# Performance work log

Measured on AMD Instinct MI355X. Metric: run time of the kernel, lower is better.

The kernel has to match this reference:

```python
import jax, jax.numpy as jnp
from jax import lax
import numpy as np

# Surrogate spike: heaviside forward, fast-sigmoid surrogate gradient (standard SNN choice).
_SURROGATE_ALPHA = 10.0

@jax.custom_vjp
def surrogate_spike(x):
    return (x > 0).astype(x.dtype)

def _ss_fwd(x):
    return (x > 0).astype(x.dtype), x

def _ss_bwd(x, g):
    return (g / (1.0 + _SURROGATE_ALPHA * jnp.abs(x)) ** 2,)

surrogate_spike.defvjp(_ss_fwd, _ss_bwd)

B, C, T, R, TIME_BINS = 256, 64, 2048, 16, 128


def setup_inputs() -> dict:
    key = jax.random.key(0)
    ks = jax.random.split(key, 8)
    return {
        "transmit_spikes": jax.random.uniform(ks[0], (B, C, T), dtype=jnp.float32),
        "receive_spikes": jax.random.uniform(ks[1], (B, 2, C, T), dtype=jnp.float32),
        "conv_w": jax.random.normal(ks[2], (R, 3), dtype=jnp.float32) * 0.5,
        "conv_b": jax.random.normal(ks[3], (R,), dtype=jnp.float32) * 0.1,
        "frequency": jnp.linspace(-1.5, 1.5, R, dtype=jnp.float32),
        "decay": jax.random.normal(ks[4], (R,), dtype=jnp.float32) * 0.5,
        "threshold": jax.random.normal(ks[5], (R,), dtype=jnp.float32) * 0.5,
        "transmit_weight": jax.random.normal(ks[6], (), dtype=jnp.float32) * 0.1,
        "receive_weight": jax.random.normal(ks[7], (), dtype=jnp.float32) * 0.1,
    }


def reference(transmit_spikes, receive_spikes, conv_w, conv_b,
              frequency, decay, threshold, transmit_weight, receive_weight):
    # ---- _build_traces ----
    transmit = transmit_spikes.sum(axis=1)                        # (B, T)
    left = receive_spikes[:, 0].sum(axis=1)                       # (B, T)
    right = receive_spikes[:, 1].sum(axis=1)                      # (B, T)
    receive = 0.5 * (left + right)
    azimuth = left - right
    channel_axis = jnp.linspace(-1.0, 1.0, C).reshape(1, 1, C, 1)
    elevation = (receive_spikes * channel_axis).sum(axis=(1, 2))  # (B, T)
    signed_distance = (jax.nn.softplus(receive_weight) * receive
                       - jax.nn.softplus(transmit_weight) * transmit)
    traces = jnp.stack([signed_distance, azimuth, elevation], axis=1)  # (B, 3, T)
    # adaptive_avg_pool1d(T -> TIME_BINS); T divisible by TIME_BINS -> windowed mean
    traces = traces.reshape(B, 3, TIME_BINS, T // TIME_BINS).mean(axis=-1)
    scale = jnp.maximum(jnp.abs(traces).max(axis=(1, 2), keepdims=True), 1.0)
    traces = traces / scale                                       # (B, 3, TIME_BINS)

    # ---- 1x1 conv (pointwise linear over channel dim) ----
    drive = jnp.einsum('bct,rc->brt', traces, conv_w) + conv_b[None, :, None]  # (B, R, TIME_BINS)

    freq = 0.02 + 0.18 * jax.nn.sigmoid(frequency)[None, :]   # (1, R)
    dec = 0.8 + 0.18 * jax.nn.sigmoid(decay)[None, :]
    thr = 0.35 + 0.75 * jax.nn.sigmoid(threshold)[None, :]

    # ---- resonate-and-fire scan over time ----
    def step(carry, current):
        state, velocity = carry
        velocity = dec * velocity + current - freq * state
        state = state + freq * velocity
        spikes = surrogate_spike(state - thr)
        state = state - spikes * thr
        return (state, velocity), spikes

    drive_t = jnp.moveaxis(drive, -1, 0)  # (TIME_BINS, B, R)
    init = (jnp.zeros((B, R), drive.dtype), jnp.zeros((B, R), drive.dtype))
    _, spike_trace = lax.scan(step, init, drive_t)  # (TIME_BINS, B, R)
    pooled = spike_trace.mean(axis=0)               # (B, R)
    return pooled
```

## Files before the change

### kernel.cpp

```cpp
#include <hip/hip_runtime.h>
#include <math.h>


#define NB 256
#define NC 64
#define NT 2048
#define NR 16
#define NTB 128
#define NWIN 16

__global__ __launch_bounds__(512) void crb_kernel(
    const float* __restrict__ transmit,
    const float* __restrict__ receive,
    const float* __restrict__ conv_w,
    const float* __restrict__ conv_b,
    const float* __restrict__ frequency,
    const float* __restrict__ decay,
    const float* __restrict__ threshold,
    const float* __restrict__ tw,
    const float* __restrict__ rw,
    float* __restrict__ out)
{
    const int b   = blockIdx.x;
    const int tid = threadIdx.x;
    const int t0  = tid * 4;

    __shared__ float sdw[NTB];
    __shared__ float azw[NTB];
    __shared__ float elw[NTB];
    __shared__ float red[8];
    __shared__ float s_scale;

    float ts0=0.f, ts1=0.f, ts2=0.f, ts3=0.f;
    float ls0=0.f, ls1=0.f, ls2=0.f, ls3=0.f;
    float rs0=0.f, rs1=0.f, rs2=0.f, rs3=0.f;
    float es0=0.f, es1=0.f, es2=0.f, es3=0.f;

    const float4* tp = reinterpret_cast<const float4*>(
        transmit + (size_t)b * NC * NT + t0);
    const float4* lp = reinterpret_cast<const float4*>(
        receive + ((size_t)b * 2 + 0) * NC * NT + t0);
    const float4* rp = reinterpret_cast<const float4*>(
        receive + ((size_t)b * 2 + 1) * NC * NT + t0);
    const int row = NT / 4;

    #pragma unroll 8
    for (int c = 0; c < NC; ++c) {
        const float ch = fmaf((float)c, 2.0f / 63.0f, -1.0f);
        const float4 tv = tp[c * row];
        const float4 lv = lp[c * row];
        const float4 rv = rp[c * row];
        ts0 += tv.x; ts1 += tv.y; ts2 += tv.z; ts3 += tv.w;
        ls0 += lv.x; ls1 += lv.y; ls2 += lv.z; ls3 += lv.w;
        rs0 += rv.x; rs1 += rv.y; rs2 += rv.z; rs3 += rv.w;
        es0 = fmaf(lv.x + rv.x, ch, es0);
        es1 = fmaf(lv.y + rv.y, ch, es1);
        es2 = fmaf(lv.z + rv.z, ch, es2);
        es3 = fmaf(lv.w + rv.w, ch, es3);
    }

    const float sp_tw = log1pf(expf(tw[0]));
    const float sp_rw = log1pf(expf(rw[0]));

    float sd4, az4, el4;
    {
        const float sdv0 = sp_rw * 0.5f * (ls0 + rs0) - sp_tw * ts0;
        const float sdv1 = sp_rw * 0.5f * (ls1 + rs1) - sp_tw * ts1;
        const float sdv2 = sp_rw * 0.5f * (ls2 + rs2) - sp_tw * ts2;
        const float sdv3 = sp_rw * 0.5f * (ls3 + rs3) - sp_tw * ts3;
        sd4 = ((sdv0 + sdv1) + (sdv2 + sdv3));
        az4 = ((ls0 - rs0) + (ls1 - rs1)) + ((ls2 - rs2) + (ls3 - rs3));
        el4 = (es0 + es1) + (es2 + es3);
    }
    sd4 += __shfl_xor(sd4, 1); sd4 += __shfl_xor(sd4, 2);
    az4 += __shfl_xor(az4, 1); az4 += __shfl_xor(az4, 2);
    el4 += __shfl_xor(el4, 1); el4 += __shfl_xor(el4, 2);

    if ((tid & 3) == 0) {
        const int w = tid >> 2;
        sdw[w] = sd4 * (1.0f / NWIN);
        azw[w] = az4 * (1.0f / NWIN);
        elw[w] = el4 * (1.0f / NWIN);
    }
    __syncthreads();

    float m = 0.f;
    if (tid < 3 * NTB) {
        const float v = (tid < NTB) ? sdw[tid]
                      : (tid < 2 * NTB) ? azw[tid - NTB]
                      : elw[tid - 2 * NTB];
        m = fabsf(v);
    }
    #pragma unroll
    for (int off = 32; off >= 1; off >>= 1)
        m = fmaxf(m, __shfl_xor(m, off));
    if ((tid & 63) == 0) red[tid >> 6] = m;
    __syncthreads();
    if (tid == 0) {
        float mm = red[0];
        #pragma unroll
        for (int i = 1; i < 8; ++i) mm = fmaxf(mm, red[i]);
        s_scale = fmaxf(mm, 1.0f);
    }
    __syncthreads();

    if (tid < NR) {
        const int r = tid;
        const float inv_scale = 1.0f / s_scale;
        const float w0 = conv_w[r * 3 + 0];
        const float w1 = conv_w[r * 3 + 1];
        const float w2 = conv_w[r * 3 + 2];
        const float bias = conv_b[r];
        const float fr = 0.02f + 0.18f / (1.0f + expf(-frequency[r]));
        const float dc = 0.80f + 0.18f / (1.0f + expf(-decay[r]));
        const float th = 0.35f + 0.75f / (1.0f + expf(-threshold[r]));

        float st = 0.f, vel = 0.f, cnt = 0.f;
        for (int t = 0; t < NTB; ++t) {
            const float cur =
                (sdw[t] * w0 + azw[t] * w1 + elw[t] * w2) * inv_scale + bias;
            vel = dc * vel + cur - fr * st;
            st  = st + fr * vel;
            const float sp = ((st - th) > 0.0f) ? 1.0f : 0.0f;
            st -= sp * th;
            cnt += sp;
        }
        out[(size_t)b * NR + r] = cnt * (1.0f / NTB);
    }
}

extern "C" void kernel_launch(void* const* d_in, const int* in_sizes, int n_in,
                              void* d_out, int out_size, void* d_ws, size_t ws_size,
                              hipStream_t stream) {
    const float* transmit  = (const float*)d_in[0];
    const float* receive   = (const float*)d_in[1];
    const float* conv_w    = (const float*)d_in[2];
    const float* conv_b    = (const float*)d_in[3];
    const float* frequency = (const float*)d_in[4];
    const float* decay     = (const float*)d_in[5];
    const float* threshold = (const float*)d_in[6];
    const float* tw        = (const float*)d_in[7];
    const float* rw        = (const float*)d_in[8];
    float* out = (float*)d_out;

    crb_kernel<<<NB, 512, 0, stream>>>(transmit, receive, conv_w, conv_b,
                                       frequency, decay, threshold, tw, rw, out);
}
```

Baseline: 450.7 us.

## Split channel/time reduction across many blocks with a separate scan kernel

The single fused kernel, which used one 512-thread block per batch, becomes two kernels. The first spreads the channel and time reduction over 8 blocks per batch (2048 blocks in total) and writes per-window partial sums to workspace. The second combines the partials, computes the scale and runs the resonate-and-fire scan. The goal is more memory-level parallelism and occupancy for the bandwidth-bound reduction, which previously had only 256 blocks on a 256-CU device. The cost is an extra launch and a small workspace round-trip.

```diff
diff --git a/kernel.cpp b/kernel.cpp
--- a/kernel.cpp
+++ b/kernel.cpp
@@ -8,10 +8,72 @@
 #define NR 16
 #define NTB 128
 #define NWIN 16
+#define CS 4
+#define TS 2
+#define CCH (NC / CS)
+#define TCH (NT / TS)
+#define WCH (TCH / NWIN)
 
-__global__ __launch_bounds__(512) void crb_kernel(
+__global__ __launch_bounds__(256) void crb_reduce_k1(
     const float* __restrict__ transmit,
     const float* __restrict__ receive,
+    float* __restrict__ part)
+{
+    const int blk  = blockIdx.x;
+    const int b    = blk / (TS * CS);
+    const int rem  = blk % (TS * CS);
+    const int ts_i = rem / CS;
+    const int cs_i = rem % CS;
+    const int tid  = threadIdx.x;
+    const int t0   = ts_i * TCH + tid * 4;
+    const int c0   = cs_i * CCH;
+
+    const float4* tp = reinterpret_cast<const float4*>(
+        transmit + ((size_t)b * NC + c0) * NT + t0);
+    const float4* lp = reinterpret_cast<const float4*>(
+        receive + (((size_t)b * 2 + 0) * NC + c0) * NT + t0);
+    const float4* rp = reinterpret_cast<const float4*>(
+        receive + (((size_t)b * 2 + 1) * NC + c0) * NT + t0);
+    const int row = NT / 4;
+
+    float ts0=0.f, ts1=0.f, ts2=0.f, ts3=0.f;
+    float ls0=0.f, ls1=0.f, ls2=0.f, ls3=0.f;
+    float rs0=0.f, rs1=0.f, rs2=0.f, rs3=0.f;
+    float es0=0.f, es1=0.f, es2=0.f, es3=0.f;
+
+    #pragma unroll 8
+    for (int i = 0; i < CCH; ++i) {
+        const float ch = fmaf((float)(c0 + i), 2.0f / 63.0f, -1.0f);
+        const float4 tv = tp[i * row];
+        const float4 lv = lp[i * row];
+        const float4 rv = rp[i * row];
+        ts0 += tv.x; ts1 += tv.y; ts2 += tv.z; ts3 += tv.w;
+        ls0 += lv.x; ls1 += lv.y; ls2 += lv.z; ls3 += lv.w;
+        rs0 += rv.x; rs1 += rv.y; rs2 += rv.z; rs3 += rv.w;
+        es0 = fmaf(lv.x + rv.x, ch, es0);
+        es1 = fmaf(lv.y + rv.y, ch, es1);
+        es2 = fmaf(lv.z + rv.z, ch, es2);
+        es3 = fmaf(lv.w + rv.w, ch, es3);
+    }
+
+    float t4 = (ts0 + ts1) + (ts2 + ts3);
+    float l4 = (ls0 + ls1) + (ls2 + ls3);
+    float r4 = (rs0 + rs1) + (rs2 + rs3);
+    float e4 = (es0 + es1) + (es2 + es3);
+
+    t4 += __shfl_xor(t4, 1); t4 += __shfl_xor(t4, 2);
+    l4 += __shfl_xor(l4, 1); l4 += __shfl_xor(l4, 2);
+    r4 += __shfl_xor(r4, 1); r4 += __shfl_xor(r4, 2);
+    e4 += __shfl_xor(e4, 1); e4 += __shfl_xor(e4, 2);
+
+    const int q = tid & 3;
+    const int w = ts_i * WCH + (tid >> 2);
+    const float v = (q == 0) ? t4 : (q == 1) ? l4 : (q == 2) ? r4 : e4;
+    part[(((size_t)b * 4 + q) * NTB + w) * CS + cs_i] = v;
+}
+
+__global__ __launch_bounds__(128) void crb_scan_k2(
+    const float* __restrict__ part,
     const float* __restrict__ conv_w,
     const float* __restrict__ conv_b,
     const float* __restrict__ frequency,
@@ -23,85 +85,41 @@
 {
     const int b   = blockIdx.x;
     const int tid = threadIdx.x;
-    const int t0  = tid * 4;
 
     __shared__ float sdw[NTB];
     __shared__ float azw[NTB];
     __shared__ float elw[NTB];
-    __shared__ float red[8];
+    __shared__ float red[2];
     __shared__ float s_scale;
 
-    float ts0=0.f, ts1=0.f, ts2=0.f, ts3=0.f;
-    float ls0=0.f, ls1=0.f, ls2=0.f, ls3=0.f;
-    float rs0=0.f, rs1=0.f, rs2=0.f, rs3=0.f;
-    float es0=0.f, es1=0.f, es2=0.f, es3=0.f;
-
-    const float4* tp = reinterpret_cast<const float4*>(
-        transmit + (size_t)b * NC * NT + t0);
-    const float4* lp = reinterpret_cast<const float4*>(
-        receive + ((size_t)b * 2 + 0) * NC * NT + t0);
-    const float4* rp = reinterpret_cast<const float4*>(
-        receive + ((size_t)b * 2 + 1) * NC * NT + t0);
-    const int row = NT / 4;
-
-    #pragma unroll 8
-    for (int c = 0; c < NC; ++c) {
-        const float ch = fmaf((float)c, 2.0f / 63.0f, -1.0f);
-        const float4 tv = tp[c * row];
-        const float4 lv = lp[c * row];
-        const float4 rv = rp[c * row];
-        ts0 += tv.x; ts1 += tv.y; ts2 += tv.z; ts3 += tv.w;
-        ls0 += lv.x; ls1 += lv.y; ls2 += lv.z; ls3 += lv.w;
-        rs0 += rv.x; rs1 += rv.y; rs2 += rv.z; rs3 += rv.w;
-        es0 = fmaf(lv.x + rv.x, ch, es0);
-        es1 = fmaf(lv.y + rv.y, ch, es1);
-        es2 = fmaf(lv.z + rv.z, ch, es2);
-        es3 = fmaf(lv.w + rv.w, ch, es3);
-    }
+    const float4 tq = *reinterpret_cast<const float4*>(
+        &part[(((size_t)b * 4 + 0) * NTB + tid) * CS]);
+    const float4 lq = *reinterpret_cast<const float4*>(
+        &part[(((size_t)b * 4 + 1) * NTB + tid) * CS]);
+    const float4 rq = *reinterpret_cast<const float4*>(
+        &part[(((size_t)b * 4 + 2) * NTB + tid) * CS]);
+    const float4 eq = *reinterpret_cast<const float4*>(
+        &part[(((size_t)b * 4 + 3) * NTB + tid) * CS]);
+    const float tsum = ((tq.x + tq.y) + (tq.z + tq.w));
+    const float lsum = ((lq.x + lq.y) + (lq.z + lq.w));
+    const float rsum = ((rq.x + rq.y) + (rq.z + rq.w));
+    const float esum = ((eq.x + eq.y) + (eq.z + eq.w));
 
     const float sp_tw = log1pf(expf(tw[0]));
     const float sp_rw = log1pf(expf(rw[0]));
 
-    float sd4, az4, el4;
-    {
-        const float sdv0 = sp_rw * 0.5f * (ls0 + rs0) - sp_tw * ts0;
-        const float sdv1 = sp_rw * 0.5f * (ls1 + rs1) - sp_tw * ts1;
-        const float sdv2 = sp_rw * 0.5f * (ls2 + rs2) - sp_tw * ts2;
-        const float sdv3 = sp_rw * 0.5f * (ls3 + rs3) - sp_tw * ts3;
-        sd4 = ((sdv0 + sdv1) + (sdv2 + sdv3));
-        az4 = ((ls0 - rs0) + (ls1 - rs1)) + ((ls2 - rs2) + (ls3 - rs3));
-        el4 = (es0 + es1) + (es2 + es3);
-    }
-    sd4 += __shfl_xor(sd4, 1); sd4 += __shfl_xor(sd4, 2);
-    az4 += __shfl_xor(az4, 1); az4 += __shfl_xor(az4, 2);
-    el4 += __shfl_xor(el4, 1); el4 += __shfl_xor(el4, 2);
+    const float sd = (sp_rw * 0.5f * (lsum + rsum) - sp_tw * tsum) * (1.0f / NWIN);
+    const float az = (lsum - rsum) * (1.0f / NWIN);
+    const float el = esum * (1.0f / NWIN);
+    sdw[tid] = sd; azw[tid] = az; elw[tid] = el;
 
-    if ((tid & 3) == 0) {
-        const int w = tid >> 2;
-        sdw[w] = sd4 * (1.0f / NWIN);
-        azw[w] = az4 * (1.0f / NWIN);
-        elw[w] = el4 * (1.0f / NWIN);
-    }
-    __syncthreads();
-
-    float m = 0.f;
-    if (tid < 3 * NTB) {
-        const float v = (tid < NTB) ? sdw[tid]
-                      : (tid < 2 * NTB) ? azw[tid - NTB]
-                      : elw[tid - 2 * NTB];
-        m = fabsf(v);
-    }
+    float m = fmaxf(fabsf(sd), fmaxf(fabsf(az), fabsf(el)));
     #pragma unroll
     for (int off = 32; off >= 1; off >>= 1)
         m = fmaxf(m, __shfl_xor(m, off));
     if ((tid & 63) == 0) red[tid >> 6] = m;
     __syncthreads();
-    if (tid == 0) {
-        float mm = red[0];
-        #pragma unroll
-        for (int i = 1; i < 8; ++i) mm = fmaxf(mm, red[i]);
-        s_scale = fmaxf(mm, 1.0f);
-    }
+    if (tid == 0) s_scale = fmaxf(fmaxf(red[0], red[1]), 1.0f);
     __syncthreads();
 
     if (tid < NR) {
@@ -141,8 +159,10 @@
     const float* threshold = (const float*)d_in[6];
     const float* tw        = (const float*)d_in[7];
     const float* rw        = (const float*)d_in[8];
-    float* out = (float*)d_out;
+    float* out  = (float*)d_out;
+    float* part = (float*)d_ws;
 
-    crb_kernel<<<NB, 512, 0, stream>>>(transmit, receive, conv_w, conv_b,
-                                       frequency, decay, threshold, tw, rw, out);
+    crb_reduce_k1<<<NB * TS * CS, 256, 0, stream>>>(transmit, receive, part);
+    crb_scan_k2<<<NB, 128, 0, stream>>>(part, conv_w, conv_b, frequency,
+                                        decay, threshold, tw, rw, out);
 }
```

Result: no change. 454.1 us (+0.8%).
